# Kernel optimization log

Hardware: AMD Instinct MI355X
Metric: run time of the kernel (lower is better)

The kernel has to match this reference:

```python
import jax, jax.numpy as jnp
import numpy as np

B, S, H, NH = 4, 2048, 1024, 16
HD = H // NH

def setup_inputs() -> dict:
    key = jax.random.key(0)
    ks = jax.random.split(key, 11)
    std = 1.0 / np.sqrt(H)
    inp = {
        'query': jax.random.normal(ks[0], (B, S, H), dtype=jnp.float32),
        'key':   jax.random.normal(ks[1], (B, S, H), dtype=jnp.float32),
        'value': jax.random.normal(ks[2], (B, S, H), dtype=jnp.float32),
        'Wq': jax.random.uniform(ks[3], (H, H), jnp.float32, -std, std),
        'bq': jax.random.uniform(ks[4], (H,), jnp.float32, -std, std),
        'Wk': jax.random.uniform(ks[5], (H, H), jnp.float32, -std, std),
        'bk': jax.random.uniform(ks[6], (H,), jnp.float32, -std, std),
        'Wv': jax.random.uniform(ks[7], (H, H), jnp.float32, -std, std),
        'bv': jax.random.uniform(ks[8], (H,), jnp.float32, -std, std),
        'Wo': jax.random.uniform(ks[9], (H, H), jnp.float32, -std, std),
        'bo': jax.random.uniform(ks[10], (H,), jnp.float32, -std, std),
    }
    return inp

def reference(query, key, value, Wq, bq, Wk, bk, Wv, bv, Wo, bo):
    def split_heads(x):  # [B,S,H] -> [B,NH,S,HD]
        return x.reshape(B, -1, NH, HD).transpose(0, 2, 1, 3)
    Q = split_heads(query @ Wq.T + bq)
    K = split_heads(key @ Wk.T + bk)
    V = split_heads(value @ Wv.T + bv)
    scores = jnp.einsum('bhqd,bhkd->bhqk', Q, K) / np.sqrt(HD).astype(np.float32)
    weights = jax.nn.softmax(scores, axis=-1)
    attn = jnp.einsum('bhqk,bhkd->bhqd', weights, V)  # [B,NH,S,HD]
    attn = attn.transpose(0, 2, 1, 3).reshape(B, -1, H)
    return attn @ Wo.T + bo
```

## Files before the change

### kernel.cpp

```cpp
#include <hip/hip_runtime.h>
#include <hip/hip_bf16.h>

typedef __attribute__((ext_vector_type(4)))  float f32x4;
typedef __attribute__((ext_vector_type(16))) float f32x16;
typedef __attribute__((ext_vector_type(8)))  short bf16x8;
typedef __attribute__((ext_vector_type(4)))  short bf16x4;

#define DEVI static __device__ __forceinline__
#define WAITV(N) asm volatile("s_waitcnt vmcnt(" #N ")" ::: "memory")
#define BAR() __builtin_amdgcn_s_barrier()
#define SCHEDB() __builtin_amdgcn_sched_barrier(0)

constexpr int Bn = 4, Sn = 2048, Hn = 1024, NHn = 16, HDn = 64;
constexpr int Kn = 1024, Nn = 1024;
constexpr float QSCALE = 0.18033688011112042f;

DEVI unsigned short f2bf(float x) {
    union { float f; unsigned u; } v; v.f = x;
    unsigned r = v.u + 0x7fffu + ((v.u >> 16) & 1u);
    return (unsigned short)(r >> 16);
}

DEVI f32x4 mfma16(bf16x8 a, bf16x8 b, f32x4 c) {
    return __builtin_amdgcn_mfma_f32_16x16x32_bf16(a, b, c, 0, 0, 0);
}
DEVI f32x16 mfma32(bf16x8 a, bf16x8 b, f32x16 c) {
    return __builtin_amdgcn_mfma_f32_32x32x16_bf16(a, b, c, 0, 0, 0);
}
DEVI unsigned cvt_pk_bf16(float lo, float hi) {
    unsigned r;
    asm("v_cvt_pk_bf16_f32 %0, %1, %2" : "=v"(r) : "v"(lo), "v"(hi));
    return r;
}
DEVI void pl32swap(unsigned &a, unsigned &b) {
    asm("v_permlane32_swap_b32 %0, %1" : "+v"(a), "+v"(b));
}
DEVI float exp2_raw(float x) { return __builtin_amdgcn_exp2f(x); }

typedef const __attribute__((address_space(1))) void* gas1_t;
typedef __attribute__((address_space(3))) void* gas3_t;

__global__ void convert_w_kernel(const float* __restrict__ w0, const float* __restrict__ w1,
                                 const float* __restrict__ w2, const float* __restrict__ w3,
                                 unsigned short* __restrict__ out)
{
    int mat = blockIdx.x >> 10;
    int i4  = ((blockIdx.x & 1023) << 8) + threadIdx.x;
    const float* w = mat == 0 ? w0 : mat == 1 ? w1 : mat == 2 ? w2 : w3;
    f32x4 v = *reinterpret_cast<const f32x4*>(w + (size_t)i4 * 4);
    union { unsigned u[2]; bf16x4 s; } pk;
    pk.u[0] = cvt_pk_bf16(v[0], v[1]);
    pk.u[1] = cvt_pk_bf16(v[2], v[3]);
    *reinterpret_cast<bf16x4*>(out + (((size_t)mat) << 20) + (size_t)i4 * 4) = pk.s;
}

__global__ __launch_bounds__(256, 2)
void out_proj_kernel(const unsigned short* __restrict__ Aw, const unsigned short* __restrict__ Bw,
                     const float* __restrict__ bias, float* __restrict__ Out)
{
    __shared__ __align__(16) unsigned short As[128 * 32];
    __shared__ __align__(16) unsigned short Bs[128 * 32];

    const int tid = threadIdx.x;
    const int wid = tid >> 6, lane = tid & 63;
    const int lhi = lane >> 4, llo = lane & 15;
    const int bid = blockIdx.x;
    const int sid = (bid & 7) * 64 + (bid >> 3);
    const int bx = sid & 7, by = sid >> 3;
    const int brow = by * 128, bcol = bx * 128;
    const int wr = wid >> 1, wc = wid & 1;

    f32x4 acc[4][4] = {};

    for (int kt = 0; kt < Kn / 32; ++kt) {
        __syncthreads();
        #pragma unroll
        for (int r = 0; r < 2; ++r) {
            int lin = r * 256 + tid;
            int row = lin >> 2, kc = (lin & 3) * 8;
            __builtin_amdgcn_global_load_lds(
                (gas1_t)(Bw + (size_t)(bcol + row) * Kn + kt * 32 + kc),
                (gas3_t)(Bs + (size_t)(r * 256 + wid * 64) * 8), 16, 0, 0);
        }
        #pragma unroll
        for (int r = 0; r < 2; ++r) {
            int lin = r * 256 + tid;
            int row = lin >> 2, kc = (lin & 3) * 8;
            __builtin_amdgcn_global_load_lds(
                (gas1_t)(Aw + (size_t)(brow + row) * Kn + kt * 32 + kc),
                (gas3_t)(As + (size_t)(r * 256 + wid * 64) * 8), 16, 0, 0);
        }
        __syncthreads();

        bf16x8 a[4], b[4];
        #pragma unroll
        for (int m = 0; m < 4; ++m)
            a[m] = *reinterpret_cast<const bf16x8*>(As + (wr * 64 + m * 16 + llo) * 32 + lhi * 8);
        #pragma unroll
        for (int n = 0; n < 4; ++n)
            b[n] = *reinterpret_cast<const bf16x8*>(Bs + (wc * 64 + n * 16 + llo) * 32 + lhi * 8);
        #pragma unroll
        for (int m = 0; m < 4; ++m)
            #pragma unroll
            for (int n = 0; n < 4; ++n)
                acc[m][n] = mfma16(a[m], b[n], acc[m][n]);
    }

    #pragma unroll
    for (int m = 0; m < 4; ++m)
        #pragma unroll
        for (int n = 0; n < 4; ++n) {
            const int col  = bcol + wc * 64 + n * 16 + llo;
            const int row0 = brow + wr * 64 + m * 16 + lhi * 4;
            const float bv = bias[col];
            #pragma unroll
            for (int r = 0; r < 4; ++r)
                Out[(size_t)(row0 + r) * Nn + col] = acc[m][n][r] + bv;
        }
}

__global__ __launch_bounds__(256, 4)
void qkv_proj_kernel(const float* __restrict__ xq, const float* __restrict__ xk,
                     const float* __restrict__ xv, const unsigned short* __restrict__ Wb,
                     const float* __restrict__ bq, const float* __restrict__ bk,
                     const float* __restrict__ bv,
                     unsigned short* __restrict__ Qw, unsigned short* __restrict__ Kw,
                     unsigned short* __restrict__ Vw)
{
    __shared__ __align__(16) unsigned short As[2][128 * 32];
    __shared__ __align__(16) unsigned short Bs[2][128 * 32];

    const int z = blockIdx.z;
    const float* A           = z == 0 ? xq : z == 1 ? xk : xv;
    const unsigned short* W  = Wb + (((size_t)z) << 20);
    const float* bias        = z == 0 ? bq : z == 1 ? bk : bv;
    unsigned short* Out      = z == 0 ? Qw : z == 1 ? Kw : Vw;
    const float scale        = z == 0 ? QSCALE : 1.0f;

    const int tid = threadIdx.x;
    const int wid = tid >> 6, lane = tid & 63;
    const int lhi = lane >> 4, llo = lane & 15;
    const int bid = blockIdx.x;
    const int sid = (bid & 7) * 64 + (bid >> 3);
    const int bx = sid & 7, by = sid >> 3;
    const int brow = by * 128, bcol = bx * 128;
    const int wr = wid >> 1, wc = wid & 1;

    const int aBase = (brow + (tid >> 3)) * Kn + (tid & 7) * 4;
    const int bBase = (bcol + (tid >> 2)) * Kn + (tid & 3) * 8;
    const int aLds  = (tid >> 3) * 32 + (tid & 7) * 4;
    unsigned short* const bLds = Bs[0] + (size_t)(wid * 64) * 8;

    f32x4 acc[4][4] = {};
    f32x4 ar[4];

    auto issueA = [&](int kt) {
        #pragma unroll
        for (int r = 0; r < 4; ++r)
            ar[r] = *reinterpret_cast<const f32x4*>(A + (size_t)(aBase + r * 32 * Kn + kt * 32));
    };
    auto stageB = [&](int buf, int kt) {
        #pragma unroll
        for (int r = 0; r < 2; ++r)
            __builtin_amdgcn_global_load_lds(
                (gas1_t)(W + (size_t)(bBase + r * 64 * Kn + kt * 32)),
                (gas3_t)(bLds + buf * 4096 + r * 2048), 16, 0, 0);
    };
    auto writeA = [&](int buf) {
        #pragma unroll
        for (int r = 0; r < 4; ++r) {
            union { unsigned u[2]; bf16x4 s; } pk;
            pk.u[0] = cvt_pk_bf16(ar[r][0], ar[r][1]);
            pk.u[1] = cvt_pk_bf16(ar[r][2], ar[r][3]);
            *reinterpret_cast<bf16x4*>(As[buf] + aLds + r * 1024) = pk.s;
        }
    };
    auto compute = [&](int buf) {
        bf16x8 a[4], b[4];
        #pragma unroll
        for (int m = 0; m < 4; ++m)
            a[m] = *reinterpret_cast<const bf16x8*>(As[buf] + (wr * 64 + llo) * 32 + lhi * 8 + m * 512);
        #pragma unroll
        for (int n = 0; n < 4; ++n)
            b[n] = *reinterpret_cast<const bf16x8*>(Bs[buf] + (wc * 64 + llo) * 32 + lhi * 8 + n * 512);
        #pragma unroll
        for (int m = 0; m < 4; ++m)
            #pragma unroll
            for (int n = 0; n < 4; ++n)
                acc[m][n] = mfma16(a[m], b[n], acc[m][n]);
    };

    constexpr int NKT = Kn / 32;
    issueA(0);
    stageB(0, 0);
    writeA(0);
    __syncthreads();

    for (int kt = 0; kt < NKT; kt += 2) {
        issueA(kt + 1);
        stageB(1, kt + 1);
        compute(0);
        writeA(1);
        __syncthreads();
        if (kt + 2 < NKT) { issueA(kt + 2); stageB(0, kt + 2); }
        compute(1);
        if (kt + 2 < NKT) writeA(0);
        __syncthreads();
    }

    #pragma unroll
    for (int m = 0; m < 4; ++m) {
        #pragma unroll
        for (int n = 0; n < 4; ++n) {
            const int col  = bcol + wc * 64 + n * 16 + llo;
            const int row0 = brow + wr * 64 + m * 16 + lhi * 4;
            const float bv = bias[col];
            const int hh = col >> 6, d = col & 63;
            if (z != 2) {
                unsigned short* O = (unsigned short*)Out;
                #pragma unroll
                for (int r = 0; r < 4; ++r) {
                    int rowm = row0 + r;
                    int bb = rowm >> 11, ss = rowm & 2047;
                    O[((((size_t)bb * NHn + hh) * Sn + ss) << 6) + d] =
                        f2bf((acc[m][n][r] + bv) * scale);
                }
            } else {
                unsigned short* O = (unsigned short*)Out;
                const int bb = row0 >> 11, ss = row0 & 2047;
                union { unsigned u[2]; bf16x4 s; } pk;
                pk.u[0] = cvt_pk_bf16(acc[m][n][0] + bv, acc[m][n][1] + bv);
                pk.u[1] = cvt_pk_bf16(acc[m][n][2] + bv, acc[m][n][3] + bv);
                *reinterpret_cast<bf16x4*>(O + (((size_t)bb * NHn + hh) * HDn + d) * Sn + ss) = pk.s;
            }
        }
    }
}

__global__ __launch_bounds__(256, 2)
void attn_kernel(const unsigned short* __restrict__ Q, const unsigned short* __restrict__ K,
                 const unsigned short* __restrict__ Vt, unsigned short* __restrict__ On)
{
    __shared__ __align__(16) unsigned short LDST[3 * 8192];

    const int tid = threadIdx.x;
    const int wid = tid >> 6, lane = tid & 63;
    const int l31 = lane & 31, h = lane >> 5;
    const int bid = blockIdx.x;
    const int sid = (bid & 7) * 64 + (bid >> 3);
    const int bh = sid >> 3;
    const int qt = sid & 7;
    const int q0 = qt * 256 + wid * 64;

    const unsigned short* Qb = Q + (size_t)bh * Sn * HDn;
    const unsigned short* Kb = K + (size_t)bh * Sn * HDn;
    const unsigned short* Vb = Vt + (size_t)bh * HDn * Sn;

    int koff[2], voff[2];
    #pragma unroll
    for (int r = 0; r < 2; ++r) {
        int lin = (r * 256 + tid) * 16;
        int row = lin >> 7, colb = lin & 127;
        int scolb = colb ^ ((row & 7) << 4);
        koff[r] = row * HDn + (scolb >> 1);
        voff[r] = row * Sn + (scolb >> 1);
    }

    auto stage = [&](int bufEl, int key0) {
        #pragma unroll
        for (int r = 0; r < 2; ++r)
            __builtin_amdgcn_global_load_lds((gas1_t)(Kb + koff[r] + key0 * HDn),
                (gas3_t)(LDST + bufEl + r * 2048 + wid * 512), 16, 0, 0);
        #pragma unroll
        for (int r = 0; r < 2; ++r)
            __builtin_amdgcn_global_load_lds((gas1_t)(Vb + voff[r] + key0),
                (gas3_t)(LDST + bufEl + 4096 + r * 2048 + wid * 512), 16, 0, 0);
    };
    auto rdT = [&](int byteoff) -> bf16x8 {
        return *reinterpret_cast<const bf16x8*>((const char*)LDST + byteoff);
    };
    const int lrow = l31 * 128;
    const int lswz = (l31 & 7) << 4;

    bf16x8 qfA[4], qfB[4];
    #pragma unroll
    for (int sd = 0; sd < 4; ++sd) {
        qfA[sd] = *reinterpret_cast<const bf16x8*>(Qb + (size_t)(q0 + l31) * HDn + sd * 16 + h * 8);
        qfB[sd] = *reinterpret_cast<const bf16x8*>(Qb + (size_t)(q0 + 32 + l31) * HDn + sd * 16 + h * 8);
    }

    f32x16 oA0 = {}, oA1 = {}, oB0 = {}, oB1 = {};
    float lA = 0.f, lB = 0.f;

    auto body = [&](int base) {
        bf16x8 ka0[4], ka1[4];
        #pragma unroll
        for (int sd = 0; sd < 4; ++sd) {
            int la = lrow + ((sd * 32 + h * 16) ^ lswz);
            ka0[sd] = rdT(base + la);
            ka1[sd] = rdT(base + 4096 + la);
        }
        f32x16 sA0 = {}, sA1 = {}, sB0 = {}, sB1 = {};
        __builtin_amdgcn_s_setprio(1);
        #pragma unroll
        for (int sd = 0; sd < 4; ++sd) sA0 = mfma32(ka0[sd], qfA[sd], sA0);
        #pragma unroll
        for (int sd = 0; sd < 4; ++sd) sA1 = mfma32(ka1[sd], qfA[sd], sA1);
        #pragma unroll
        for (int sd = 0; sd < 4; ++sd) sB0 = mfma32(ka0[sd], qfB[sd], sB0);
        #pragma unroll
        for (int sd = 0; sd < 4; ++sd) sB1 = mfma32(ka1[sd], qfB[sd], sB1);
        __builtin_amdgcn_s_setprio(0);

        bf16x8 va0[4], va1[4];
        #pragma unroll
        for (int S = 0; S < 4; ++S) {
            int la = lrow + ((S * 32 + h * 16) ^ lswz);
            va0[S] = rdT(base + 8192 + la);
            va1[S] = rdT(base + 8192 + 4096 + la);
        }

        #pragma unroll
        for (int r = 0; r < 16; ++r) {
            sA0[r] = exp2_raw(sA0[r]); sA1[r] = exp2_raw(sA1[r]);
            sB0[r] = exp2_raw(sB0[r]); sB1[r] = exp2_raw(sB1[r]);
        }

        {
            float sa[16], sb[16];
            #pragma unroll
            for (int r = 0; r < 16; ++r) { sa[r] = sA0[r] + sA1[r]; sb[r] = sB0[r] + sB1[r]; }
            #pragma unroll
            for (int st = 8; st > 0; st >>= 1)
                #pragma unroll
                for (int r = 0; r < 8; ++r)
                    if (r < st) { sa[r] += sa[r + st]; sb[r] += sb[r + st]; }
            lA += sa[0];
            lB += sb[0];
        }

        unsigned WpA[2][4][2], WpB[2][4][2];
        #pragma unroll
        for (int R = 0; R < 4; ++R) {
            WpA[0][R][0] = cvt_pk_bf16(sA0[4 * R],     sA0[4 * R + 1]);
            WpA[0][R][1] = cvt_pk_bf16(sA0[4 * R + 2], sA0[4 * R + 3]);
            WpA[1][R][0] = cvt_pk_bf16(sA1[4 * R],     sA1[4 * R + 1]);
            WpA[1][R][1] = cvt_pk_bf16(sA1[4 * R + 2], sA1[4 * R + 3]);
            WpB[0][R][0] = cvt_pk_bf16(sB0[4 * R],     sB0[4 * R + 1]);
            WpB[0][R][1] = cvt_pk_bf16(sB0[4 * R + 2], sB0[4 * R + 3]);
            WpB[1][R][0] = cvt_pk_bf16(sB1[4 * R],     sB1[4 * R + 1]);
            WpB[1][R][1] = cvt_pk_bf16(sB1[4 * R + 2], sB1[4 * R + 3]);
        }

        #pragma unroll
        for (int kc = 0; kc < 2; ++kc) {
            #pragma unroll
            for (int sp = 0; sp < 2; ++sp) {
                const int S = kc * 2 + sp;
                unsigned a0 = WpA[kc][2 * sp][0], a2 = WpA[kc][2 * sp + 1][0];
                unsigned a1 = WpA[kc][2 * sp][1], a3 = WpA[kc][2 * sp + 1][1];
                pl32swap(a0, a2);
                pl32swap(a1, a3);
                union { unsigned u[4]; bf16x8 v; } pbA;
                pbA.u[0] = a0; pbA.u[1] = a1; pbA.u[2] = a2; pbA.u[3] = a3;
                unsigned b0 = WpB[kc][2 * sp][0], b2 = WpB[kc][2 * sp + 1][0];
                unsigned b1 = WpB[kc][2 * sp][1], b3 = WpB[kc][2 * sp + 1][1];
                pl32swap(b0, b2);
                pl32swap(b1, b3);
                union { unsigned u[4]; bf16x8 v; } pbB;
                pbB.u[0] = b0; pbB.u[1] = b1; pbB.u[2] = b2; pbB.u[3] = b3;
                __builtin_amdgcn_s_setprio(1);
                oA0 = mfma32(va0[S], pbA.v, oA0);
                oA1 = mfma32(va1[S], pbA.v, oA1);
                oB0 = mfma32(va0[S], pbB.v, oB0);
                oB1 = mfma32(va1[S], pbB.v, oB1);
                __builtin_amdgcn_s_setprio(0);
            }
        }
    };

    constexpr int NT = Sn / 64;
    stage(0, 0);
    int ec = 0, en = 8192, e2 = 16384;
    for (int n = 0; n < NT; ++n) {
        if (n + 1 < NT) {
            stage(en, (n + 1) * 64);
            WAITV(4);
        } else {
            WAITV(0);
        }
        BAR(); SCHEDB();
        body(ec * 2);
        int t = ec; ec = en; en = e2; e2 = t;
    }

    lA += __shfl_xor(lA, 32, 64);
    lB += __shfl_xor(lB, 32, 64);
    const float invA = 1.f / lA, invB = 1.f / lB;
    const int b = bh >> 4, hh = bh & 15;
    unsigned short* OrowA = On + ((size_t)b * Sn + (q0 + l31))      * Hn + hh * 64;
    unsigned short* OrowB = On + ((size_t)b * Sn + (q0 + 32 + l31)) * Hn + hh * 64;
    #pragma unroll
    for (int g = 0; g < 4; ++g) {
        union { unsigned u[2]; bf16x4 s; } pA0, pA1, pB0, pB1;
        pA0.u[0] = cvt_pk_bf16(oA0[4 * g] * invA,     oA0[4 * g + 1] * invA);
        pA0.u[1] = cvt_pk_bf16(oA0[4 * g + 2] * invA, oA0[4 * g + 3] * invA);
        pA1.u[0] = cvt_pk_bf16(oA1[4 * g] * invA,     oA1[4 * g + 1] * invA);
        pA1.u[1] = cvt_pk_bf16(oA1[4 * g + 2] * invA, oA1[4 * g + 3] * invA);
        pB0.u[0] = cvt_pk_bf16(oB0[4 * g] * invB,     oB0[4 * g + 1] * invB);
        pB0.u[1] = cvt_pk_bf16(oB0[4 * g + 2] * invB, oB0[4 * g + 3] * invB);
        pB1.u[0] = cvt_pk_bf16(oB1[4 * g] * invB,     oB1[4 * g + 1] * invB);
        pB1.u[1] = cvt_pk_bf16(oB1[4 * g + 2] * invB, oB1[4 * g + 3] * invB);
        *reinterpret_cast<bf16x4*>(OrowA + g * 8 + 4 * h)      = pA0.s;
        *reinterpret_cast<bf16x4*>(OrowA + 32 + g * 8 + 4 * h) = pA1.s;
        *reinterpret_cast<bf16x4*>(OrowB + g * 8 + 4 * h)      = pB0.s;
        *reinterpret_cast<bf16x4*>(OrowB + 32 + g * 8 + 4 * h) = pB1.s;
    }
}

extern "C" void kernel_launch(void* const* d_in, const int* in_sizes, int n_in,
                              void* d_out, int out_size, void* d_ws, size_t ws_size,
                              hipStream_t stream)
{
    (void)in_sizes; (void)n_in; (void)out_size;
    const float* q  = (const float*)d_in[0];
    const float* k  = (const float*)d_in[1];
    const float* v  = (const float*)d_in[2];
    const float* Wq = (const float*)d_in[3];
    const float* bq = (const float*)d_in[4];
    const float* Wk = (const float*)d_in[5];
    const float* bk = (const float*)d_in[6];
    const float* Wv = (const float*)d_in[7];
    const float* bv = (const float*)d_in[8];
    const float* Wo = (const float*)d_in[9];
    const float* bo = (const float*)d_in[10];
    float* out = (float*)d_out;

    if (ws_size < (size_t)72 * 1024 * 1024) return;

    unsigned short* Wb = (unsigned short*)d_ws;
    unsigned short* Qw = Wb + (size_t)4 * 1024 * 1024;
    unsigned short* Kw = Qw + (size_t)8 * 1024 * 1024;
    unsigned short* Vw = Kw + (size_t)8 * 1024 * 1024;
    unsigned short* Aw = Vw + (size_t)8 * 1024 * 1024;

    convert_w_kernel<<<4096, 256, 0, stream>>>(Wq, Wk, Wv, Wo, Wb);
    qkv_proj_kernel<<<dim3(512, 1, 3), 256, 0, stream>>>(q, k, v, Wb, bq, bk, bv, Qw, Kw, Vw);
    attn_kernel<<<512, 256, 0, stream>>>(Qw, Kw, Vw, Aw);
    out_proj_kernel<<<512, 256, 0, stream>>>(Aw, Wb + ((size_t)3 << 20), bo, out);
}
```

Before: 192.0 us.

## Double-buffer out_proj and widen K tile to 64 in projection GEMMs

The output projection GEMM moves from a single-buffered K=32 loop with two barriers per step to a double-buffered K=64 pipeline that prefetches the next tile while computing the current one. The QKV projection kernel also doubles its K tile to 64, halving the number of barrier-separated iterations, and lowers its launch-bounds occupancy hint from 4 to 2 blocks. Both kernels now use a doubled shared-memory footprint, which may reduce occupancy and introduce LDS bank conflicts with the 128-byte row stride.

After: 205.4 us. +7.0%, slower.

```diff
diff --git a/kernel.cpp b/kernel.cpp
--- a/kernel.cpp
+++ b/kernel.cpp
@@ -58,8 +58,8 @@
 void out_proj_kernel(const unsigned short* __restrict__ Aw, const unsigned short* __restrict__ Bw,
                      const float* __restrict__ bias, float* __restrict__ Out)
 {
-    __shared__ __align__(16) unsigned short As[128 * 32];
-    __shared__ __align__(16) unsigned short Bs[128 * 32];
+    __shared__ __align__(16) unsigned short As[2][128 * 64];
+    __shared__ __align__(16) unsigned short Bs[2][128 * 64];
 
     const int tid = threadIdx.x;
     const int wid = tid >> 6, lane = tid & 63;
@@ -70,40 +70,49 @@
     const int brow = by * 128, bcol = bx * 128;
     const int wr = wid >> 1, wc = wid & 1;
 
+    const int trow = tid >> 3, tcol = (tid & 7) * 8;
+    const int aBase = (brow + trow) * Kn + tcol;
+    const int bBase = (bcol + trow) * Kn + tcol;
+
     f32x4 acc[4][4] = {};
 
-    for (int kt = 0; kt < Kn / 32; ++kt) {
+    auto stage = [&](int buf, int kt) {
+        #pragma unroll
+        for (int r = 0; r < 4; ++r)
+            __builtin_amdgcn_global_load_lds(
+                (gas1_t)(Bw + (size_t)(bBase + r * 32 * Kn + kt * 64)),
+                (gas3_t)(Bs[buf] + (size_t)(r * 256 + wid * 64) * 8), 16, 0, 0);
+        #pragma unroll
+        for (int r = 0; r < 4; ++r)
+            __builtin_amdgcn_global_load_lds(
+                (gas1_t)(Aw + (size_t)(aBase + r * 32 * Kn + kt * 64)),
+                (gas3_t)(As[buf] + (size_t)(r * 256 + wid * 64) * 8), 16, 0, 0);
+    };
+    auto compute = [&](int buf) {
+        #pragma unroll
+        for (int kk = 0; kk < 2; ++kk) {
+            bf16x8 a[4], b[4];
+            #pragma unroll
+            for (int m = 0; m < 4; ++m)
+                a[m] = *reinterpret_cast<const bf16x8*>(As[buf] + (wr * 64 + m * 16 + llo) * 64 + kk * 32 + lhi * 8);
+            #pragma unroll
+            for (int n = 0; n < 4; ++n)
+                b[n] = *reinterpret_cast<const bf16x8*>(Bs[buf] + (wc * 64 + n * 16 + llo) * 64 + kk * 32 + lhi * 8);
+            #pragma unroll
+            for (int m = 0; m < 4; ++m)
+                #pragma unroll
+                for (int n = 0; n < 4; ++n)
+                    acc[m][n] = mfma16(a[m], b[n], acc[m][n]);
+        }
+    };
+
+    constexpr int NKT = Kn / 64;
+    stage(0, 0);
+    __syncthreads();
+    for (int kt = 0; kt < NKT; ++kt) {
+        if (kt + 1 < NKT) stage((kt + 1) & 1, kt + 1);
+        compute(kt & 1);
         __syncthreads();
-        #pragma unroll
-        for (int r = 0; r < 2; ++r) {
-            int lin = r * 256 + tid;
-            int row = lin >> 2, kc = (lin & 3) * 8;
-            __builtin_amdgcn_global_load_lds(
-                (gas1_t)(Bw + (size_t)(bcol + row) * Kn + kt * 32 + kc),
-                (gas3_t)(Bs + (size_t)(r * 256 + wid * 64) * 8), 16, 0, 0);
-        }
-        #pragma unroll
-        for (int r = 0; r < 2; ++r) {
-            int lin = r * 256 + tid;
-            int row = lin >> 2, kc = (lin & 3) * 8;
-            __builtin_amdgcn_global_load_lds(
-                (gas1_t)(Aw + (size_t)(brow + row) * Kn + kt * 32 + kc),
-                (gas3_t)(As + (size_t)(r * 256 + wid * 64) * 8), 16, 0, 0);
-        }
-        __syncthreads();
-
-        bf16x8 a[4], b[4];
-        #pragma unroll
-        for (int m = 0; m < 4; ++m)
-            a[m] = *reinterpret_cast<const bf16x8*>(As + (wr * 64 + m * 16 + llo) * 32 + lhi * 8);
-        #pragma unroll
-        for (int n = 0; n < 4; ++n)
-            b[n] = *reinterpret_cast<const bf16x8*>(Bs + (wc * 64 + n * 16 + llo) * 32 + lhi * 8);
-        #pragma unroll
-        for (int m = 0; m < 4; ++m)
-            #pragma unroll
-            for (int n = 0; n < 4; ++n)
-                acc[m][n] = mfma16(a[m], b[n], acc[m][n]);
     }
 
     #pragma unroll
@@ -119,7 +128,7 @@
         }
 }
 
-__global__ __launch_bounds__(256, 4)
+__global__ __launch_bounds__(256, 2)
 void qkv_proj_kernel(const float* __restrict__ xq, const float* __restrict__ xk,
                      const float* __restrict__ xv, const unsigned short* __restrict__ Wb,
                      const float* __restrict__ bq, const float* __restrict__ bk,
@@ -127,8 +136,8 @@
                      unsigned short* __restrict__ Qw, unsigned short* __restrict__ Kw,
                      unsigned short* __restrict__ Vw)
 {
-    __shared__ __align__(16) unsigned short As[2][128 * 32];
-    __shared__ __align__(16) unsigned short Bs[2][128 * 32];
+    __shared__ __align__(16) unsigned short As[2][128 * 64];
+    __shared__ __align__(16) unsigned short Bs[2][128 * 64];
 
     const int z = blockIdx.z;
     const float* A           = z == 0 ? xq : z == 1 ? xk : xv;
@@ -146,29 +155,30 @@
     const int brow = by * 128, bcol = bx * 128;
     const int wr = wid >> 1, wc = wid & 1;
 
-    const int aBase = (brow + (tid >> 3)) * Kn + (tid & 7) * 4;
-    const int bBase = (bcol + (tid >> 2)) * Kn + (tid & 3) * 8;
-    const int aLds  = (tid >> 3) * 32 + (tid & 7) * 4;
-    unsigned short* const bLds = Bs[0] + (size_t)(wid * 64) * 8;
+    const int arow = tid >> 4, acol = (tid & 15) * 4;
+    const int aBase = (brow + arow) * Kn + acol;
+    const int aLds  = arow * 64 + acol;
+    const int brw = tid >> 3, bcl = (tid & 7) * 8;
+    const int bBase = (bcol + brw) * Kn + bcl;
 
     f32x4 acc[4][4] = {};
-    f32x4 ar[4];
+    f32x4 ar[8];
 
     auto issueA = [&](int kt) {
         #pragma unroll
+        for (int r = 0; r < 8; ++r)
+            ar[r] = *reinterpret_cast<const f32x4*>(A + (size_t)(aBase + r * 16 * Kn + kt * 64));
+    };
+    auto stageB = [&](int buf, int kt) {
+        #pragma unroll
         for (int r = 0; r < 4; ++r)
-            ar[r] = *reinterpret_cast<const f32x4*>(A + (size_t)(aBase + r * 32 * Kn + kt * 32));
-    };
-    auto stageB = [&](int buf, int kt) {
-        #pragma unroll
-        for (int r = 0; r < 2; ++r)
             __builtin_amdgcn_global_load_lds(
-                (gas1_t)(W + (size_t)(bBase + r * 64 * Kn + kt * 32)),
-                (gas3_t)(bLds + buf * 4096 + r * 2048), 16, 0, 0);
+                (gas1_t)(W + (size_t)(bBase + r * 32 * Kn + kt * 64)),
+                (gas3_t)(Bs[buf] + (size_t)(r * 256 + wid * 64) * 8), 16, 0, 0);
     };
     auto writeA = [&](int buf) {
         #pragma unroll
-        for (int r = 0; r < 4; ++r) {
+        for (int r = 0; r < 8; ++r) {
             union { unsigned u[2]; bf16x4 s; } pk;
             pk.u[0] = cvt_pk_bf16(ar[r][0], ar[r][1]);
             pk.u[1] = cvt_pk_bf16(ar[r][2], ar[r][3]);
@@ -176,21 +186,24 @@
         }
     };
     auto compute = [&](int buf) {
-        bf16x8 a[4], b[4];
-        #pragma unroll
-        for (int m = 0; m < 4; ++m)
-            a[m] = *reinterpret_cast<const bf16x8*>(As[buf] + (wr * 64 + llo) * 32 + lhi * 8 + m * 512);
-        #pragma unroll
-        for (int n = 0; n < 4; ++n)
-            b[n] = *reinterpret_cast<const bf16x8*>(Bs[buf] + (wc * 64 + llo) * 32 + lhi * 8 + n * 512);
-        #pragma unroll
-        for (int m = 0; m < 4; ++m)
+        #pragma unroll
+        for (int kk = 0; kk < 2; ++kk) {
+            bf16x8 a[4], b[4];
+            #pragma unroll
+            for (int m = 0; m < 4; ++m)
+                a[m] = *reinterpret_cast<const bf16x8*>(As[buf] + (wr * 64 + m * 16 + llo) * 64 + kk * 32 + lhi * 8);
             #pragma unroll
             for (int n = 0; n < 4; ++n)
-                acc[m][n] = mfma16(a[m], b[n], acc[m][n]);
-    };
-
-    constexpr int NKT = Kn / 32;
+                b[n] = *reinterpret_cast<const bf16x8*>(Bs[buf] + (wc * 64 + n * 16 + llo) * 64 + kk * 32 + lhi * 8);
+            #pragma unroll
+            for (int m = 0; m < 4; ++m)
+                #pragma unroll
+                for (int n = 0; n < 4; ++n)
+                    acc[m][n] = mfma16(a[m], b[n], acc[m][n]);
+        }
+    };
+
+    constexpr int NKT = Kn / 64;
     issueA(0);
     stageB(0, 0);
     writeA(0);
```
